# Optimization experiments

Hardware: AMD Instinct MI355X
Metric: run time of the kernel (lower is better)

## Reference

```python
import jax, jax.numpy as jnp
import numpy as np

T, B, D, H = 64, 512, 768, 12
HD = D // H
EPS = 1e-8  # torch cosine_similarity eps


def setup_inputs() -> dict:
    key = jax.random.key(0)
    k0, k1, k2, k3 = jax.random.split(key, 4)
    node_embs = jax.random.normal(k0, (T, B, D), dtype=jnp.float32)
    in_proj_w = jax.random.normal(k1, (3 * D, D), dtype=jnp.float32) * 0.02
    in_proj_b = jnp.zeros((3 * D,), dtype=jnp.float32)
    out_proj_w = jax.random.normal(k2, (D, D), dtype=jnp.float32) * 0.02
    out_proj_b = jnp.zeros((D,), dtype=jnp.float32)
    return {"node_embs": node_embs, "in_proj_w": in_proj_w, "in_proj_b": in_proj_b,
            "out_proj_w": out_proj_w, "out_proj_b": out_proj_b}


def reference(node_embs, in_proj_w, in_proj_b, out_proj_w, out_proj_b):
    # node_embs: (T, B, D). Original loops over t calling MHA on (B, 1, D)
    # i.e. self-attention across the B axis with batch=1, fused here over T.
    qkv = jnp.einsum('tbd,ed->tbe', node_embs, in_proj_w) + in_proj_b  # (T, B, 3D)
    q, k, v = jnp.split(qkv, 3, axis=-1)

    def heads(x):  # (T, B, D) -> (T, H, B, HD)
        return x.reshape(T, B, H, HD).transpose(0, 2, 1, 3)

    q, k, v = heads(q), heads(k), heads(v)
    scores = jnp.einsum('thqd,thkd->thqk', q, k) / np.sqrt(HD).astype(np.float32)
    attn = jax.nn.softmax(scores, axis=-1)
    ctx = jnp.einsum('thqk,thkd->thqd', attn, v)  # (T, H, B, HD)
    ctx = ctx.transpose(0, 2, 1, 3).reshape(T, B, D)
    out = jnp.einsum('tbd,ed->tbe', ctx, out_proj_w) + out_proj_b  # (T, B, D)

    # cosine similarity between all pairs over B, then mean over first index
    norm = jnp.maximum(jnp.linalg.norm(out, axis=-1), EPS)  # (T, B)
    xn = out / norm[..., None]
    sim = jnp.einsum('tid,tjd->tij', xn, xn)  # (T, B, B)
    adj = sim.mean(axis=1)[..., None]  # (T, B, 1) == (T, B, N) with N=1
    return adj
```

## Files before the change

kernel.cpp:

```cpp
#include <hip/hip_runtime.h>

#define T_ 64
#define B_ 512
#define D_ 768
#define H_ 12
#define HD_ 64
#define M1 (T_*B_)
#define N_QKV (3*D_)

typedef __attribute__((ext_vector_type(8))) short short8;
typedef __attribute__((ext_vector_type(4))) float f32x4;

__device__ __forceinline__ unsigned short f2b(float f) {
  unsigned int u = __float_as_uint(f);
  u = (u + 0x7FFFu + ((u >> 16) & 1u)) >> 16;
  return (unsigned short)u;
}
__device__ __forceinline__ float b2f(unsigned short s) {
  return __uint_as_float(((unsigned int)s) << 16);
}

__device__ __forceinline__ void load_lds16(const unsigned short* g, unsigned short* l) {
  __builtin_amdgcn_global_load_lds(
      (const __attribute__((address_space(1))) unsigned int*)g,
      (__attribute__((address_space(3))) unsigned int*)l, 16, 0, 0);
}

#define N4_NODE 6291456
#define N4_WQKV 442368
#define N4_WOUT 147456
__global__ __launch_bounds__(256) void k_cast_all(
    const float* __restrict__ node, const float* __restrict__ wqkv,
    const float* __restrict__ wout, unsigned short* __restrict__ x_bf,
    unsigned short* __restrict__ wqkv_bf, unsigned short* __restrict__ wout_bf) {
  int i = blockIdx.x * 256 + threadIdx.x;
  const float* src; unsigned short* dst; int off;
  if (i < N4_NODE)                 { src = node; dst = x_bf;    off = i; }
  else if (i < N4_NODE + N4_WQKV)  { src = wqkv; dst = wqkv_bf; off = i - N4_NODE; }
  else                             { src = wout; dst = wout_bf; off = i - N4_NODE - N4_WQKV; }
  float4 v = ((const float4*)src)[off];
  ushort4 o;
  o.x = f2b(v.x); o.y = f2b(v.y); o.z = f2b(v.z); o.w = f2b(v.w);
  ((ushort4*)dst)[off] = o;
}

#define SB0() __builtin_amdgcn_sched_barrier(0)
#define BARF() do { SB0(); __builtin_amdgcn_s_barrier(); SB0(); } while (0)
#define WLG0() asm volatile("s_waitcnt lgkmcnt(0)" ::: "memory")
#define WVM8() asm volatile("s_waitcnt vmcnt(8)" ::: "memory")
#define WVM6() asm volatile("s_waitcnt vmcnt(6)" ::: "memory")
#define WVM4() asm volatile("s_waitcnt vmcnt(4)" ::: "memory")
#define WVM2() asm volatile("s_waitcnt vmcnt(2)" ::: "memory")
#define WVM0() asm volatile("s_waitcnt vmcnt(0)" ::: "memory")

#define STG_A(SLOT, GOFF) do { \
  load_lds16(Ag + (GOFF),          lds + (SLOT)*16384 + tid*8); \
  load_lds16(Ag + 98304 + (GOFF),  lds + (SLOT)*16384 + 4096 + tid*8); \
} while (0)
#define STG_B(SLOT, GOFF) do { \
  load_lds16(Bg0 + (GOFF),          lds + (SLOT)*16384 + 8192 + tid*8); \
  load_lds16(Bg0 + 98304 + (GOFF),  lds + (SLOT)*16384 + 12288 + tid*8); \
} while (0)

#define RD_ALO(PAR, SLOT) do { \
  const unsigned short* p_ = lds + (SLOT)*16384 + aBase; \
  aLo[PAR][0] = *(const short8*)(p_); \
  aLo[PAR][1] = *(const short8*)(p_ + 512); \
  aLo[PAR][2] = *(const short8*)(p_ + 1024); \
  aLo[PAR][3] = *(const short8*)(p_ + 1536); \
} while (0)

#define RD_BHI(SLOT) do { \
  const unsigned short* pb_ = lds + (SLOT)*16384 + bBase; \
  bC[0] = *(const short8*)(pb_); \
  bC[1] = *(const short8*)(pb_ + 512); \
  bC[2] = *(const short8*)(pb_ + 1024); \
  bC[3] = *(const short8*)(pb_ + 1536); \
  const unsigned short* pa_ = lds + (SLOT)*16384 + aBase + 2048; \
  aHi[0] = *(const short8*)(pa_); \
  aHi[1] = *(const short8*)(pa_ + 512); \
  aHi[2] = *(const short8*)(pa_ + 1024); \
  aHi[3] = *(const short8*)(pa_ + 1536); \
} while (0)

#define MM_LO(PAR) do { \
  __builtin_amdgcn_s_setprio(1); \
  _Pragma("unroll") \
  for (int mf = 0; mf < 4; mf++) \
    _Pragma("unroll") \
    for (int nf = 0; nf < 4; nf++) \
      acc[mf][nf] = __builtin_amdgcn_mfma_f32_16x16x32_bf16(aLo[PAR][mf], bC[nf], acc[mf][nf], 0, 0, 0); \
  __builtin_amdgcn_s_setprio(0); \
} while (0)

#define MM_HI() do { \
  __builtin_amdgcn_s_setprio(1); \
  _Pragma("unroll") \
  for (int mf = 0; mf < 4; mf++) \
    _Pragma("unroll") \
    for (int nf = 0; nf < 4; nf++) \
      acc[4+mf][nf] = __builtin_amdgcn_mfma_f32_16x16x32_bf16(aHi[mf], bC[nf], acc[4+mf][nf], 0, 0, 0); \
  __builtin_amdgcn_s_setprio(0); \
} while (0)

#define P0(SLOT, PAR, SSLOT, GOFF, WVSTMT) do { \
  RD_BHI(SLOT); STG_A(SSLOT, GOFF); WVSTMT; BARF(); WLG0(); MM_LO(PAR); BARF(); \
} while (0)
#define P1(NPAR, NSLOT, SSLOT, GOFF) do { \
  RD_ALO(NPAR, NSLOT); STG_B(SSLOT, GOFF); BARF(); MM_HI(); BARF(); \
} while (0)

#define GEMM_RING_KLOOP(Aptr, Bptr) \
  const int tid = threadIdx.x; \
  const int lane = tid & 63, wave = tid >> 6; \
  const int ln = lane & 15, quad = lane >> 4; \
  const int wm = wave & 1, wn = wave >> 1; \
   \
  const int w_ = tid & 7, g_ = tid >> 3; \
  const int rowS_ = ((g_ >> 2) << 3) + (w_ & 4) + (g_ & 3); \
  const int octS_ = (w_ & 3) ^ (g_ & 3); \
  const unsigned short* Ag = Aptr + (size_t)(m0 + rowS_)*768 + octS_*8; \
  const unsigned short* Bg0 = Bptr + (size_t)(n0 + rowS_)*768 + octS_*8; \
   \
  const int inner_ = (((ln>>3)*4 + (ln&3))*8 + ((ln&7) ^ quad)) * 8; \
  const int aBase = wm*4096 + inner_; \
  const int bBase = 8192 + (wn>>1)*4096 + (wn&1)*2048 + inner_; \
  short8 aLo[2][4], aHi[4], bC[4]; \
  f32x4 acc[8][4] = {}; \
  STG_A(0, 0); STG_B(0, 0); STG_A(1, 32); STG_B(1, 32); STG_A(2, 64); STG_B(2, 64); \
  WVM8(); BARF(); \
  RD_ALO(0, 0); \
   \
  P0(0, 0, 3, 96, WVM6()); \
  P1(1, 1, 3, 96); \
  for (int J = 0; J < 5; ++J) { \
    P0(1, 1, 0, 128, WVM6()); \
    P1(0, 2, 0, 128); \
    P0(2, 0, 1, 160, WVM6()); \
    P1(1, 3, 1, 160); \
    P0(3, 1, 2, 192, WVM6()); \
    P1(0, 0, 2, 192); \
    P0(0, 0, 3, 224, WVM6()); \
    P1(1, 1, 3, 224); \
    Ag += 128; Bg0 += 128; \
  } \
   \
  RD_BHI(1); WVM4(); BARF(); WLG0(); MM_LO(1); BARF(); \
  RD_ALO(0, 2); BARF(); MM_HI(); BARF(); \
  RD_BHI(2); WVM0(); BARF(); WLG0(); MM_LO(0); BARF(); \
  RD_ALO(1, 3); BARF(); MM_HI(); BARF(); \
  RD_BHI(3); BARF(); WLG0(); MM_LO(1); BARF(); \
  MM_HI(); \
  __syncthreads();

__global__ __launch_bounds__(512, 2) void k_gemm_qkv8(
    const unsigned short* __restrict__ A,
    const unsigned short* __restrict__ Bw,
    const float* __restrict__ bias,
    unsigned short* __restrict__ qo,
    unsigned short* __restrict__ ko,
    unsigned short* __restrict__ vTo)
{
  extern __shared__ __align__(16) unsigned short lds[];
  const int bb = blockIdx.x;
  const int xcd = bb & 7, idx = bb >> 3;
  const int m0 = (xcd*16 + idx/9) * 256;
  const int n0 = (idx%9) * 256;
  GEMM_RING_KLOOP(A, Bw)

  const int t = m0 >> 9, mb = m0 & 511;
  if (n0 < 1536) {
    unsigned short* dst = (n0 < 768) ? qo : ko;
    const int colbase = (n0 < 768) ? n0 : n0 - 768;
#pragma unroll
    for (int half = 0; half < 2; half++) {
      __syncthreads();
      if (wm == half) {
#pragma unroll
        for (int nf = 0; nf < 4; nf++) {
          const int col = wn*64 + nf*16 + ln;
          const float bi = bias[n0 + col];
          const int cc = col >> 3, cs = col & 7;
#pragma unroll
          for (int mf = 0; mf < 8; mf++) {
            const int row = mf*16 + quad*4;
#pragma unroll
            for (int r = 0; r < 4; r++) {
              const int rw = row + r;
              lds[rw*256 + ((cc ^ (rw&7))<<3) + cs] = f2b(acc[mf][nf][r] + bi);
            }
          }
        }
      }
      __syncthreads();
#pragma unroll
      for (int it = 0; it < 8; it++) {
        int ci = it*512 + tid;
        int r2 = ci >> 5, cj = ci & 31;
        int within = colbase + cj*8;
        int h = within >> 6, hd = within & 63;
        *(uint4*)&dst[((size_t)(t*H_ + h)*B_ + mb + half*128 + r2)*HD_ + hd] =
            *(const uint4*)&lds[r2*256 + ((cj ^ (r2&7))<<3)];
      }
    }
  } else {
#pragma unroll
    for (int ch = 0; ch < 2; ch++) {
      __syncthreads();
      if ((wn >> 1) == ch) {
#pragma unroll
        for (int nf = 0; nf < 4; nf++) {
          const int col = wn*64 + nf*16 + ln;
          const int cl = col & 127;
          const float bi = bias[n0 + col];
#pragma unroll
          for (int mf = 0; mf < 8; mf++) {
            const int row = wm*128 + mf*16 + quad*4;
            ushort4 pk;
            pk.x = f2b(acc[mf][nf][0] + bi);
            pk.y = f2b(acc[mf][nf][1] + bi);
            pk.z = f2b(acc[mf][nf][2] + bi);
            pk.w = f2b(acc[mf][nf][3] + bi);
            *(ushort4*)&lds[cl*256 + (((row>>3) ^ (cl&7))<<3) + (row&7)] = pk;
          }
        }
      }
      __syncthreads();
#pragma unroll
      for (int it = 0; it < 8; it++) {
        int ci = it*512 + tid;
        int r2 = ci >> 5, cj = ci & 31;
        int cg = (n0 - 1536) + ch*128 + r2;
        int h = cg >> 6, hd = cg & 63;
        *(uint4*)&vTo[((size_t)(t*H_ + h)*HD_ + hd)*B_ + mb + cj*8] =
            *(const uint4*)&lds[r2*256 + ((cj ^ (r2&7))<<3)];
      }
    }
  }
}

__global__ __launch_bounds__(512, 2) void k_gemm_out8(
    const unsigned short* __restrict__ A,
    const unsigned short* __restrict__ Bw,
    const float* __restrict__ bias,
    unsigned short* __restrict__ outb)
{
  extern __shared__ __align__(16) unsigned short lds[];
  const int bb = blockIdx.x;
  const int xcd = bb & 7, idx = bb >> 3;
  const int m0 = (xcd*16 + idx/3) * 256;
  const int n0 = (idx%3) * 256;
  GEMM_RING_KLOOP(A, Bw)

#pragma unroll
  for (int half = 0; half < 2; half++) {
    __syncthreads();
    if (wm == half) {
#pragma unroll
      for (int nf = 0; nf < 4; nf++) {
        const int col = wn*64 + nf*16 + ln;
        const float bi = bias[n0 + col];
        const int cc = col >> 3, cs = col & 7;
#pragma unroll
        for (int mf = 0; mf < 8; mf++) {
          const int row = mf*16 + quad*4;
#pragma unroll
          for (int r = 0; r < 4; r++) {
            const int rw = row + r;
            lds[rw*256 + ((cc ^ (rw&7))<<3) + cs] = f2b(acc[mf][nf][r] + bi);
          }
        }
      }
    }
    __syncthreads();
#pragma unroll
    for (int it = 0; it < 8; it++) {
      int ci = it*512 + tid;
      int r2 = ci >> 5, cj = ci & 31;
      *(uint4*)&outb[(size_t)(m0 + half*128 + r2)*768 + n0 + cj*8] =
          *(const uint4*)&lds[r2*256 + ((cj ^ (r2&7))<<3)];
    }
  }
}

__global__ __launch_bounds__(512) void k_attn(
    const unsigned short* __restrict__ q,
    const unsigned short* __restrict__ k,
    const unsigned short* __restrict__ vT,
    unsigned short* __restrict__ ctx)
{
  extern __shared__ __align__(16) unsigned short lds[];
  unsigned short* Ps = lds + 16384;
  float* Dn = (float*)(lds + 34816);
  const int tid = threadIdx.x;
  const int lane = tid & 63, wave = tid >> 6;
  const int ln = lane & 15, quad = lane >> 4;
  const int pxr = 8 * (ln >> 2);
  const int bb = blockIdx.x;
  const int xcd = bb & 7, idx = bb >> 3;
  const int th = xcd*96 + (idx >> 1);
  const int q0 = (idx & 1) * 256;
  const int t = th / H_, h = th - t*H_;
  const size_t base  = (size_t)th * (B_*HD_);
  const size_t baseT = (size_t)th * (HD_*B_);

  const int rS = tid >> 3, cS = (tid & 7) ^ (rS & 7);

  short8 qf[2][2];
#pragma unroll
  for (int s = 0; s < 2; s++) {
    const unsigned short* qp = &q[base + (size_t)(q0 + wave*32 + s*16 + ln)*HD_ + quad*8];
    qf[s][0] = *(const short8*)qp;
    qf[s][1] = *(const short8*)(qp + 32);
  }
  f32x4 acc[2][4] = {};
  float dpart[2] = {0.f, 0.f};
  unsigned short* Pw = &Ps[wave*32*72];

  load_lds16(&k[base + (size_t)(0 + rS)*HD_ + cS*8], &lds[tid*8]);
  load_lds16(&vT[baseT + (size_t)rS*B_ + 0 + cS*8], &lds[4096 + tid*8]);

  for (int it = 0; it < 8; ++it) {
    const int p = it & 1;
    unsigned short* Ks = &lds[p*8192];
    unsigned short* VTb = &lds[p*8192 + 4096];
    if (it < 7) {
      const int kt1 = (it+1)*64;
      load_lds16(&k[base + (size_t)(kt1 + rS)*HD_ + cS*8], &lds[(p^1)*8192 + tid*8]);
      load_lds16(&vT[baseT + (size_t)rS*B_ + kt1 + cS*8], &lds[(p^1)*8192 + 4096 + tid*8]);
      WVM2();
    } else {
      WVM0();
    }
    BARF();
    f32x4 sf[2][4] = {};
#pragma unroll
    for (int ki = 0; ki < 4; ki++) {
      int row = ki*16 + ln;
      short8 kf0 = *(const short8*)&Ks[row*64 + (quad     ^ (row & 7))*8];
      short8 kf1 = *(const short8*)&Ks[row*64 + ((4+quad) ^ (row & 7))*8];
#pragma unroll
      for (int s = 0; s < 2; s++) {
        sf[s][ki] = __builtin_amdgcn_mfma_f32_16x16x32_bf16(kf0, qf[s][0], sf[s][ki], 0, 0, 0);
        sf[s][ki] = __builtin_amdgcn_mfma_f32_16x16x32_bf16(kf1, qf[s][1], sf[s][ki], 0, 0, 0);
      }
    }
#pragma unroll
    for (int s = 0; s < 2; s++)
#pragma unroll
      for (int ki = 0; ki < 4; ki++) {
        float p0 = __expf(sf[s][ki][0] * 0.125f);
        float p1 = __expf(sf[s][ki][1] * 0.125f);
        float p2 = __expf(sf[s][ki][2] * 0.125f);
        float p3 = __expf(sf[s][ki][3] * 0.125f);
        dpart[s] += (p0 + p1) + (p2 + p3);
        uint2 uu;
        uu.x = (__float_as_uint(p1) & 0xFFFF0000u) | (__float_as_uint(p0) >> 16);
        uu.y = (__float_as_uint(p3) & 0xFFFF0000u) | (__float_as_uint(p2) >> 16);
        int col = (ki*16 + quad*4) ^ pxr;
        *(uint2*)&Pw[(s*16 + ln)*72 + col] = uu;
      }
    short8 pa[2][2];
#pragma unroll
    for (int s = 0; s < 2; s++)
#pragma unroll
      for (int hf = 0; hf < 2; hf++)
        pa[s][hf] = *(const short8*)&Pw[(s*16 + ln)*72 + ((hf*32 + quad*8) ^ pxr)];
#pragma unroll
    for (int ds = 0; ds < 4; ds++) {
      int row = ds*16 + ln;
      short8 vb0 = *(const short8*)&VTb[row*64 + (quad     ^ (row & 7))*8];
      short8 vb1 = *(const short8*)&VTb[row*64 + ((4+quad) ^ (row & 7))*8];
#pragma unroll
      for (int s = 0; s < 2; s++) {
        acc[s][ds] = __builtin_amdgcn_mfma_f32_16x16x32_bf16(pa[s][0], vb0, acc[s][ds], 0, 0, 0);
        acc[s][ds] = __builtin_amdgcn_mfma_f32_16x16x32_bf16(pa[s][1], vb1, acc[s][ds], 0, 0, 0);
      }
    }
    BARF();
  }
#pragma unroll
  for (int s = 0; s < 2; s++) {
    float d = dpart[s];
    d += __shfl_xor(d, 16);
    d += __shfl_xor(d, 32);
    if (quad == 0) Dn[wave*64 + s*16 + ln] = d;
  }
#pragma unroll
  for (int s = 0; s < 2; s++) {
    int qrow = q0 + wave*32 + s*16 + quad*4;
#pragma unroll
    for (int r = 0; r < 4; r++) {
      float invd = 1.f / Dn[wave*64 + s*16 + quad*4 + r];
      size_t o = ((size_t)t*B_ + (qrow + r))*D_ + h*HD_ + ln;
#pragma unroll
      for (int ds = 0; ds < 4; ds++)
        ctx[o + ds*16] = f2b(acc[s][ds][r] * invd);
    }
  }
}

__global__ __launch_bounds__(256) void k_norms1(const unsigned short* __restrict__ outb,
                                                float* __restrict__ norms,
                                                float* __restrict__ pmvec)
{
  __shared__ float wsum[4*768];
  int blk = blockIdx.x;
  int t = blk >> 3, c = blk & 7;
  int wave = threadIdx.x >> 6, lane = threadIdx.x & 63;
  float macc[12];
#pragma unroll
  for (int j = 0; j < 12; j++) macc[j] = 0.f;
  for (int i = 0; i < 16; i++) {
    int b = c*64 + wave*16 + i;
    const unsigned short* row = &outb[((size_t)t*B_ + b)*D_];
    float x[12]; float ss = 0.f;
#pragma unroll
    for (int j = 0; j < 12; j++) { x[j] = b2f(row[lane + 64*j]); ss += x[j]*x[j]; }
#pragma unroll
    for (int off = 32; off; off >>= 1) ss += __shfl_xor(ss, off);
    float nr = fmaxf(sqrtf(ss), 1e-8f);
    if (lane == 0) norms[(size_t)t*B_ + b] = nr;
    float inv = 1.f / nr;
#pragma unroll
    for (int j = 0; j < 12; j++) macc[j] += x[j]*inv;
  }
#pragma unroll
  for (int j = 0; j < 12; j++) wsum[wave*768 + 64*j + lane] = macc[j];
  __syncthreads();
  for (int d = threadIdx.x; d < 768; d += 256) {
    pmvec[(size_t)blk*768 + d] = wsum[d] + wsum[768 + d] + wsum[1536 + d] + wsum[2304 + d];
  }
}

__global__ __launch_bounds__(256) void k_norms2(const float* __restrict__ pmvec,
                                                float* __restrict__ mvec)
{
  int t = blockIdx.x;
  for (int d = threadIdx.x; d < 768; d += 256) {
    float s = 0.f;
#pragma unroll
    for (int c = 0; c < 8; c++) s += pmvec[(size_t)(t*8 + c)*768 + d];
    mvec[t*768 + d] = s * (1.0f/512.0f);
  }
}

__global__ __launch_bounds__(256) void k_adj(const unsigned short* __restrict__ outb,
                                             const float* __restrict__ norms,
                                             const float* __restrict__ mvec,
                                             float* __restrict__ adj)
{
  int idx = blockIdx.x*4 + (threadIdx.x >> 6);
  int lane = threadIdx.x & 63;
  int t = idx >> 9;
  const unsigned short* row = &outb[(size_t)idx*768];
  const float* m = &mvec[t*768];
  float dot = 0.f;
#pragma unroll
  for (int j = 0; j < 12; j++) dot += b2f(row[lane + 64*j]) * m[lane + 64*j];
#pragma unroll
  for (int off = 32; off; off >>= 1) dot += __shfl_xor(dot, off);
  if (lane == 0) adj[idx] = dot / norms[idx];
}

extern "C" void kernel_launch(void* const* d_in, const int* in_sizes, int n_in,
                              void* d_out, int out_size, void* d_ws, size_t ws_size,
                              hipStream_t stream)
{
  const float* node = (const float*)d_in[0];
  const float* wqkv = (const float*)d_in[1];
  const float* bqkv = (const float*)d_in[2];
  const float* wout = (const float*)d_in[3];
  const float* bout = (const float*)d_in[4];
  float* adj = (float*)d_out;

  char* ws = (char*)d_ws;
  const size_t SZ = (size_t)M1*D_*2;
  unsigned short* q_bf    = (unsigned short*)(ws);
  unsigned short* k_bf    = (unsigned short*)(ws + SZ);
  unsigned short* vT_bf   = (unsigned short*)(ws + 2*SZ);
  unsigned short* ctx_bf  = (unsigned short*)(ws + 3*SZ);
  unsigned short* x_bf    = (unsigned short*)(ws + 4*SZ);
  unsigned short* wqkv_bf = (unsigned short*)(ws + 5*SZ);
  unsigned short* wout_bf = (unsigned short*)(ws + 5*SZ + 3538944);
  unsigned short* out_bf  = (unsigned short*)(ws);
  float* pmvec            = (float*)(ws + 4*SZ);
  float* norms            = (float*)(ws + 5*SZ + 3538944 + 1179648);
  float* mvec             = (float*)(ws + 5*SZ + 3538944 + 1179648 + 131072);

  static int shmem_set = 0;
  if (!shmem_set) {
    hipFuncSetAttribute((const void*)k_gemm_qkv8,
                        hipFuncAttributeMaxDynamicSharedMemorySize, 131072);
    hipFuncSetAttribute((const void*)k_gemm_out8,
                        hipFuncAttributeMaxDynamicSharedMemorySize, 131072);
    hipFuncSetAttribute((const void*)k_attn,
                        hipFuncAttributeMaxDynamicSharedMemorySize, 71680);
    shmem_set = 1;
  }

  k_cast_all<<<26880, 256, 0, stream>>>(node, wqkv, wout, x_bf, wqkv_bf, wout_bf);
  k_gemm_qkv8<<<1152, 512, 131072, stream>>>(x_bf, wqkv_bf, bqkv, q_bf, k_bf, vT_bf);
  k_attn<<<1536, 512, 71680, stream>>>(q_bf, k_bf, vT_bf, ctx_bf);
  k_gemm_out8<<<384, 512, 131072, stream>>>(ctx_bf, wout_bf, bout, out_bf);
  k_norms1<<<T_*8, 256, 0, stream>>>(out_bf, norms, pmvec);
  k_norms2<<<T_, 256, 0, stream>>>(pmvec, mvec);
  k_adj<<<M1/4, 256, 0, stream>>>(out_bf, norms, mvec, adj);
}
```

Measured before the change: 448.2 us.

## Retile output-projection GEMM to 128x256 tiles with a 4-slot single-barrier ring

The output projection GEMM moves from 256x256 tiles with 384 blocks to 128x256 tiles with 768 blocks, so it fills the 256 CUs more evenly. Its k-loop is rewritten as a 4-slot ring with one barrier per k-step: each step stages A and two B halves, reads all fragments, and issues 16 MFMAs. LDS use drops to 96 KB and the accumulator count halves. In exchange, each block gets less reuse of the A/B data it loads, and the pipeline has fewer separate phases to overlap loads with compute.

Measured after the change: 435.5 us. 2.8% less time.

```diff
diff --git a/kernel.cpp b/kernel.cpp
--- a/kernel.cpp
+++ b/kernel.cpp
@@ -50,6 +50,7 @@
 #define WVM8() asm volatile("s_waitcnt vmcnt(8)" ::: "memory")
 #define WVM6() asm volatile("s_waitcnt vmcnt(6)" ::: "memory")
 #define WVM4() asm volatile("s_waitcnt vmcnt(4)" ::: "memory")
+#define WVM3() asm volatile("s_waitcnt vmcnt(3)" ::: "memory")
 #define WVM2() asm volatile("s_waitcnt vmcnt(2)" ::: "memory")
 #define WVM0() asm volatile("s_waitcnt vmcnt(0)" ::: "memory")
 
@@ -115,13 +116,11 @@
   const int lane = tid & 63, wave = tid >> 6; \
   const int ln = lane & 15, quad = lane >> 4; \
   const int wm = wave & 1, wn = wave >> 1; \
-   \
   const int w_ = tid & 7, g_ = tid >> 3; \
   const int rowS_ = ((g_ >> 2) << 3) + (w_ & 4) + (g_ & 3); \
   const int octS_ = (w_ & 3) ^ (g_ & 3); \
   const unsigned short* Ag = Aptr + (size_t)(m0 + rowS_)*768 + octS_*8; \
   const unsigned short* Bg0 = Bptr + (size_t)(n0 + rowS_)*768 + octS_*8; \
-   \
   const int inner_ = (((ln>>3)*4 + (ln&3))*8 + ((ln&7) ^ quad)) * 8; \
   const int aBase = wm*4096 + inner_; \
   const int bBase = 8192 + (wn>>1)*4096 + (wn&1)*2048 + inner_; \
@@ -130,7 +129,6 @@
   STG_A(0, 0); STG_B(0, 0); STG_A(1, 32); STG_B(1, 32); STG_A(2, 64); STG_B(2, 64); \
   WVM8(); BARF(); \
   RD_ALO(0, 0); \
-   \
   P0(0, 0, 3, 96, WVM6()); \
   P1(1, 1, 3, 96); \
   for (int J = 0; J < 5; ++J) { \
@@ -144,7 +142,6 @@
     P1(1, 1, 3, 224); \
     Ag += 128; Bg0 += 128; \
   } \
-   \
   RD_BHI(1); WVM4(); BARF(); WLG0(); MM_LO(1); BARF(); \
   RD_ALO(0, 2); BARF(); MM_HI(); BARF(); \
   RD_BHI(2); WVM0(); BARF(); WLG0(); MM_LO(0); BARF(); \
@@ -239,6 +236,36 @@
   }
 }
 
+#define STG7(SLOT, GOFF) do { \
+  load_lds16(Ag + (GOFF),  lds + (SLOT)*12288 + tid*8); \
+  load_lds16(Bg0 + (GOFF), lds + (SLOT)*12288 + 4096 + tid*8); \
+  load_lds16(Bg1 + (GOFF), lds + (SLOT)*12288 + 8192 + tid*8); \
+} while (0)
+
+#define RD7(GU) do { \
+  const unsigned short* ga_ = lds + (GU)*12288; \
+  aF[0] = *(const short8*)(ga_ + aBase); \
+  aF[1] = *(const short8*)(ga_ + aBase + 512); \
+  aF[2] = *(const short8*)(ga_ + aBase + 1024); \
+  aF[3] = *(const short8*)(ga_ + aBase + 1536); \
+  bF[0] = *(const short8*)(ga_ + bBase); \
+  bF[1] = *(const short8*)(ga_ + bBase + 512); \
+  bF[2] = *(const short8*)(ga_ + bBase + 1024); \
+  bF[3] = *(const short8*)(ga_ + bBase + 1536); \
+} while (0)
+
+#define MM7() do { \
+  __builtin_amdgcn_s_setprio(1); \
+  _Pragma("unroll") \
+  for (int mf = 0; mf < 4; mf++) \
+    _Pragma("unroll") \
+    for (int nf = 0; nf < 4; nf++) \
+      acc[mf][nf] = __builtin_amdgcn_mfma_f32_16x16x32_bf16(aF[mf], bF[nf], acc[mf][nf], 0, 0, 0); \
+  __builtin_amdgcn_s_setprio(0); \
+} while (0)
+
+#define PH7(GU, GOFF) do { RD7(GU); STG7(((GU)+3)&3, GOFF); WVM6(); WLG0(); MM7(); BARF(); } while (0)
+
 __global__ __launch_bounds__(512, 2) void k_gemm_out8(
     const unsigned short* __restrict__ A,
     const unsigned short* __restrict__ Bw,
@@ -248,38 +275,59 @@
   extern __shared__ __align__(16) unsigned short lds[];
   const int bb = blockIdx.x;
   const int xcd = bb & 7, idx = bb >> 3;
-  const int m0 = (xcd*16 + idx/3) * 256;
+  const int m0 = (xcd*32 + idx/3) * 128;
   const int n0 = (idx%3) * 256;
-  GEMM_RING_KLOOP(A, Bw)
-
-#pragma unroll
-  for (int half = 0; half < 2; half++) {
-    __syncthreads();
-    if (wm == half) {
-#pragma unroll
-      for (int nf = 0; nf < 4; nf++) {
-        const int col = wn*64 + nf*16 + ln;
-        const float bi = bias[n0 + col];
-        const int cc = col >> 3, cs = col & 7;
-#pragma unroll
-        for (int mf = 0; mf < 8; mf++) {
-          const int row = mf*16 + quad*4;
-#pragma unroll
-          for (int r = 0; r < 4; r++) {
-            const int rw = row + r;
-            lds[rw*256 + ((cc ^ (rw&7))<<3) + cs] = f2b(acc[mf][nf][r] + bi);
-          }
-        }
-      }
-    }
-    __syncthreads();
-#pragma unroll
-    for (int it = 0; it < 8; it++) {
-      int ci = it*512 + tid;
-      int r2 = ci >> 5, cj = ci & 31;
-      *(uint4*)&outb[(size_t)(m0 + half*128 + r2)*768 + n0 + cj*8] =
-          *(const uint4*)&lds[r2*256 + ((cj ^ (r2&7))<<3)];
-    }
+
+  const int tid = threadIdx.x;
+  const int lane = tid & 63, wave = tid >> 6;
+  const int ln = lane & 15, quad = lane >> 4;
+  const int wm = wave & 1, wn = wave >> 1;
+  const int w_ = tid & 7, g_ = tid >> 3;
+  const int rowS_ = ((g_ >> 2) << 3) + (w_ & 4) + (g_ & 3);
+  const int octS_ = (w_ & 3) ^ (g_ & 3);
+  const unsigned short* Ag = A + (size_t)(m0 + rowS_)*768 + octS_*8;
+  const unsigned short* Bg0 = Bw + (size_t)(n0 + rowS_)*768 + octS_*8;
+  const unsigned short* Bg1 = Bg0 + (size_t)128*768;
+  const int ra_ = wm*64 + ln;
+  const int aBase = ((((ra_>>3)*4 + (ra_&3))*8) + ((ra_&7) ^ quad)) * 8;
+  const int rb_ = (wn & 1)*64 + ln;
+  const int bBase = 4096 + (wn>>1)*4096 + ((((rb_>>3)*4 + (rb_&3))*8) + ((rb_&7) ^ quad)) * 8;
+  short8 aF[4], bF[4];
+  f32x4 acc[4][4] = {};
+  STG7(0, 0); STG7(1, 32); STG7(2, 64);
+  WVM6(); BARF();
+  for (int J = 0; J < 5; ++J) {
+    PH7(0, 96); PH7(1, 128); PH7(2, 160); PH7(3, 192);
+    Ag += 128; Bg0 += 128; Bg1 += 128;
+  }
+  RD7(0); STG7(3, 96); WVM6(); WLG0(); MM7(); BARF();
+  RD7(1); WVM3(); WLG0(); MM7(); BARF();
+  RD7(2); WVM0(); WLG0(); MM7(); BARF();
+  RD7(3); WLG0(); MM7();
+  __syncthreads();
+
+#pragma unroll
+  for (int nf = 0; nf < 4; nf++) {
+    const int col = wn*64 + nf*16 + ln;
+    const float bi = bias[n0 + col];
+    const int cc = col >> 3, cs = col & 7;
+#pragma unroll
+    for (int mf = 0; mf < 4; mf++) {
+      const int row = wm*64 + mf*16 + quad*4;
+#pragma unroll
+      for (int r = 0; r < 4; r++) {
+        const int rw = row + r;
+        lds[rw*256 + ((cc ^ (rw&7))<<3) + cs] = f2b(acc[mf][nf][r] + bi);
+      }
+    }
+  }
+  __syncthreads();
+#pragma unroll
+  for (int it = 0; it < 8; it++) {
+    int ci = it*512 + tid;
+    int r2 = ci >> 5, cj = ci & 31;
+    *(uint4*)&outb[(size_t)(m0 + r2)*768 + n0 + cj*8] =
+        *(const uint4*)&lds[r2*256 + ((cj ^ (r2&7))<<3)];
   }
 }
 
@@ -493,7 +541,7 @@
     hipFuncSetAttribute((const void*)k_gemm_qkv8,
                         hipFuncAttributeMaxDynamicSharedMemorySize, 131072);
     hipFuncSetAttribute((const void*)k_gemm_out8,
-                        hipFuncAttributeMaxDynamicSharedMemorySize, 131072);
+                        hipFuncAttributeMaxDynamicSharedMemorySize, 98304);
     hipFuncSetAttribute((const void*)k_attn,
                         hipFuncAttributeMaxDynamicSharedMemorySize, 71680);
     shmem_set = 1;
@@ -502,7 +550,7 @@
   k_cast_all<<<26880, 256, 0, stream>>>(node, wqkv, wout, x_bf, wqkv_bf, wout_bf);
   k_gemm_qkv8<<<1152, 512, 131072, stream>>>(x_bf, wqkv_bf, bqkv, q_bf, k_bf, vT_bf);
   k_attn<<<1536, 512, 71680, stream>>>(q_bf, k_bf, vT_bf, ctx_bf);
-  k_gemm_out8<<<384, 512, 131072, stream>>>(ctx_bf, wout_bf, bout, out_bf);
+  k_gemm_out8<<<768, 512, 98304, stream>>>(ctx_bf, wout_bf, bout, out_bf);
   k_norms1<<<T_*8, 256, 0, stream>>>(out_bf, norms, pmvec);
   k_norms2<<<T_, 256, 0, stream>>>(pmvec, mvec);
   k_adj<<<M1/4, 256, 0, stream>>>(out_bf, norms, mvec, adj);
```
